# Kernel optimization log

Measured on AMD Instinct MI355X. Metric: run time of the kernel, lower is better.

Reference implementation:

```python
import jax, jax.numpy as jnp
import numpy as np

EPS = 1e-7  # K.epsilon()


def setup_inputs() -> dict:
    key = jax.random.key(0)
    k1, k2, k3, k4 = jax.random.split(key, 4)
    B, T, S = 512, 32, 2048  # batch, time_steps, seq_len
    inputs = jax.random.normal(k1, (B, T, S), dtype=jnp.float32)
    # Keras mask (float 0/1), same shape as inputs
    mask = (jax.random.uniform(k2, (B, T, S)) < 0.8).astype(jnp.float32)
    # 'uniform' keras initializer: U(-0.05, 0.05)
    W = jax.random.uniform(k3, (S, T, T), minval=-0.05, maxval=0.05, dtype=jnp.float32)
    b = jax.random.uniform(k4, (S, T), minval=-0.05, maxval=0.05, dtype=jnp.float32)
    return {"inputs": inputs, "mask": mask, "W": W, "b": b}


def reference(inputs, mask, W, b):
    # (B,T,S) -> (B,S,T), apply mask
    x = jnp.transpose(inputs, (0, 2, 1)) * jnp.transpose(mask, (0, 2, 1))
    # per-position matmul, batched over B and S (replaces the tf.scan over batch)
    z = jnp.einsum('bst,stu->bsu', x, W) + b  # (B,S,T)
    e = jnp.exp(jnp.tanh(z))
    att = e / (jnp.sum(e, axis=2, keepdims=True) + EPS)  # softmax-like over T
    return jnp.sum(att * x, axis=1)  # (B,T)
```

## Files before the change

kernel.cpp:

```cpp
#include <hip/hip_runtime.h>

#define EPS_K 1e-7f

typedef __attribute__((ext_vector_type(8)))  short          frag8;
typedef __attribute__((ext_vector_type(16))) float          accf16;
typedef __attribute__((ext_vector_type(4)))  unsigned short us4;

__device__ __forceinline__ unsigned f2bf(float f) {
  union { float f; unsigned u; } v; v.f = f;
  unsigned u = v.u;
  u += 0x7FFFu + ((u >> 16) & 1u);
  return u >> 16;
}
__device__ __forceinline__ float bf2f(unsigned short s) {
  union { unsigned u; float f; } v; v.u = ((unsigned)s) << 16;
  return v.f;
}
__device__ __forceinline__ unsigned pk_bf16(float lo, float hi) {
  return f2bf(lo) | (f2bf(hi) << 16);
}

__global__ __launch_bounds__(256) void wbf_prep(
    const float* __restrict__ Wt, unsigned short* __restrict__ Wbf)
{
  __shared__ unsigned short tile[32 * 33];
  const int s   = blockIdx.x;
  const int tid = threadIdx.x;
  {
    const int t  = tid >> 3;
    const int uc = tid & 7;
    const float4 v = *(const float4*)(Wt + s * 1024 + t * 32 + 4 * uc);
    tile[t * 33 + 4 * uc + 0] = (unsigned short)f2bf(v.x);
    tile[t * 33 + 4 * uc + 1] = (unsigned short)f2bf(v.y);
    tile[t * 33 + 4 * uc + 2] = (unsigned short)f2bf(v.z);
    tile[t * 33 + 4 * uc + 3] = (unsigned short)f2bf(v.w);
  }
  __syncthreads();
  {
    const int u  = tid >> 3;
    const int tc = tid & 7;
    uint2 d;
    d.x = (unsigned)tile[(4 * tc + 0) * 33 + u] | ((unsigned)tile[(4 * tc + 1) * 33 + u] << 16);
    d.y = (unsigned)tile[(4 * tc + 2) * 33 + u] | ((unsigned)tile[(4 * tc + 3) * 33 + u] << 16);
    *(uint2*)(Wbf + s * 1024 + u * 32 + 4 * tc) = d;
  }
}

template <bool WBF, bool USE_WS>
__global__ __launch_bounds__(256, 5) void attn_fused(
    const float* __restrict__ inp,
    const float* __restrict__ msk,
    const float* __restrict__ Wt,
    const unsigned short* __restrict__ Wbf,
    const float* __restrict__ bias,
    float* __restrict__ part,
    float* __restrict__ out)
{
  __shared__ unsigned short x_us[32 * 512];

  const int tid = threadIdx.x;
  const int st  = blockIdx.x >> 4;
  const int bg  = blockIdx.x & 15;
  const int s0  = st * 16;

  #pragma unroll
  for (int iter = 0; iter < 2; ++iter) {
    const int idx = iter * 256 + tid;
    const int sc  = idx & 3;
    const int tb  = (idx >> 2) & 3;
    const int b   = idx >> 4;
    const float* ip = inp + ((size_t)(bg * 32 + b) * 32 + 8 * tb) * 2048 + s0 + 4 * sc;
    const float* mp = msk + ((size_t)(bg * 32 + b) * 32 + 8 * tb) * 2048 + s0 + 4 * sc;
    unsigned c32[4][4];
    #pragma unroll
    for (int j2 = 0; j2 < 4; ++j2) {
      const float4 vi0 = *(const float4*)(ip + (2 * j2)     * 2048);
      const float4 vm0 = *(const float4*)(mp + (2 * j2)     * 2048);
      const float4 vi1 = *(const float4*)(ip + (2 * j2 + 1) * 2048);
      const float4 vm1 = *(const float4*)(mp + (2 * j2 + 1) * 2048);
      c32[0][j2] = pk_bf16(vi0.x * vm0.x, vi1.x * vm1.x);
      c32[1][j2] = pk_bf16(vi0.y * vm0.y, vi1.y * vm1.y);
      c32[2][j2] = pk_bf16(vi0.z * vm0.z, vi1.z * vm1.z);
      c32[3][j2] = pk_bf16(vi0.w * vm0.w, vi1.w * vm1.w);
    }
    #pragma unroll
    for (int w = 0; w < 4; ++w) {
      const int L = tb * 16 + 4 * sc + w;
      unsigned* dst = (unsigned*)(x_us + b * 512 + ((L ^ (b & 7)) * 8));
      *(uint4*)dst = make_uint4(c32[w][0], c32[w][1], c32[w][2], c32[w][3]);
    }
  }
  __syncthreads();

  const int lane = tid & 63;
  const int wv   = tid >> 6;
  const int n    = lane & 31;
  const int h    = lane >> 5;
  const int nx   = n & 7;

  float O[16];
  #pragma unroll
  for (int r = 0; r < 16; ++r) O[r] = 0.f;

  #pragma unroll
  for (int si = 0; si < 4; ++si) {
    const int sl = wv * 4 + si;
    const int s  = s0 + sl;

    frag8 a1, a2;
    if (WBF) {
      const unsigned short* wp = Wbf + s * 1024 + n * 32 + 8 * h;
      a1 = *(const frag8*)(wp);
      a2 = *(const frag8*)(wp + 16);
    } else {
      const float* Wp = Wt + s * 1024;
      #pragma unroll
      for (int j = 0; j < 8; ++j) {
        const int t1 = 8 * h + j;
        a1[j] = (short)f2bf(Wp[t1 * 32 + n]);
        a2[j] = (short)f2bf(Wp[(t1 + 16) * 32 + n]);
      }
    }

    const frag8 b1 = *(const frag8*)(x_us + n * 512 + (((h      * 16 + sl) ^ nx) * 8));
    const frag8 b2 = *(const frag8*)(x_us + n * 512 + ((((h + 2) * 16 + sl) ^ nx) * 8));

    accf16 acc;
    #pragma unroll
    for (int g = 0; g < 4; ++g) {
      const float4 bb = *(const float4*)(bias + s * 32 + 8 * g + 4 * h);
      acc[4 * g + 0] = bb.x; acc[4 * g + 1] = bb.y;
      acc[4 * g + 2] = bb.z; acc[4 * g + 3] = bb.w;
    }
    acc = __builtin_amdgcn_mfma_f32_32x32x16_bf16(a1, b1, acc, 0, 0, 0);
    acc = __builtin_amdgcn_mfma_f32_32x32x16_bf16(a2, b2, acc, 0, 0, 0);

    float e[16];
    float ps = 0.f;
    #pragma unroll
    for (int r = 0; r < 16; ++r) {
      const float z  = acc[r];
      const float e2 = __expf(2.f * z);
      const float th = 1.f - 2.f / (e2 + 1.f);
      e[r] = __expf(th);
      ps  += e[r];
    }
    const float tot = ps + __shfl_xor(ps, 32, 64);
    const float inv = 1.f / (tot + EPS_K);

    #pragma unroll
    for (int g = 0; g < 4; ++g) {
      const us4 xv = *(const us4*)(x_us + n * 512 + (((g * 16 + sl) ^ nx) * 8) + 4 * h);
      #pragma unroll
      for (int i = 0; i < 4; ++i)
        O[4 * g + i] += e[4 * g + i] * inv * bf2f(xv[i]);
    }
  }

  __syncthreads();
  float* red = (float*)x_us;
  #pragma unroll
  for (int r = 0; r < 16; ++r) {
    const int u = (r & 3) + 8 * (r >> 2) + 4 * h;
    red[wv * 1024 + n * 32 + (u ^ n)] = O[r];
  }
  __syncthreads();

  const int q0 = tid * 4;
  float4 v;
  float* vp = (float*)&v;
  #pragma unroll
  for (int i = 0; i < 4; ++i) {
    const int q = q0 + i;
    const int b = q >> 5, u = q & 31;
    float sum = 0.f;
    #pragma unroll
    for (int w = 0; w < 4; ++w) sum += red[w * 1024 + b * 32 + (u ^ b)];
    vp[i] = sum;
  }
  if (USE_WS) {
    *(float4*)(part + (size_t)st * 16384 + bg * 1024 + q0) = v;
  } else {
    float* op = out + bg * 1024 + q0;
    #pragma unroll
    for (int i = 0; i < 4; ++i) atomicAdd(op + i, vp[i]);
  }
}

__global__ __launch_bounds__(256) void reduce_part(
    const float* __restrict__ part, float* __restrict__ out)
{
  const int f = blockIdx.x * 256 + threadIdx.x;
  float s = 0.f;
  #pragma unroll 8
  for (int st = 0; st < 128; ++st) s += part[(size_t)st * 16384 + f];
  out[f] = s;
}

extern "C" void kernel_launch(void* const* d_in, const int* in_sizes, int n_in,
                              void* d_out, int out_size, void* d_ws, size_t ws_size,
                              hipStream_t stream) {
  const float* inp  = (const float*)d_in[0];
  const float* msk  = (const float*)d_in[1];
  const float* Wt   = (const float*)d_in[2];
  const float* bias = (const float*)d_in[3];
  float* out = (float*)d_out;

  const size_t part_sz = (size_t)128 * 16384 * sizeof(float);
  const size_t wbf_sz  = (size_t)2048 * 1024 * sizeof(unsigned short);

  if (ws_size >= part_sz + wbf_sz) {
    float* part = (float*)d_ws;
    unsigned short* Wbf = (unsigned short*)((char*)d_ws + part_sz);
    wbf_prep<<<dim3(2048), dim3(256), 0, stream>>>(Wt, Wbf);
    attn_fused<true, true><<<dim3(2048), dim3(256), 0, stream>>>(
        inp, msk, Wt, Wbf, bias, part, out);
    reduce_part<<<dim3(64), dim3(256), 0, stream>>>(part, out);
  } else if (ws_size >= part_sz) {
    float* part = (float*)d_ws;
    attn_fused<false, true><<<dim3(2048), dim3(256), 0, stream>>>(
        inp, msk, Wt, nullptr, bias, part, out);
    reduce_part<<<dim3(64), dim3(256), 0, stream>>>(part, out);
  } else {
    (void)hipMemsetAsync(out, 0, (size_t)out_size * sizeof(float), stream);
    attn_fused<false, false><<<dim3(2048), dim3(256), 0, stream>>>(
        inp, msk, Wt, nullptr, bias, nullptr, out);
  }
}
```

Baseline: 311.3 us.

## Retile fused attention to 32 positions x 16 batches with 16x16x32 MFMA

Each block now covers 32 sequence positions and 16 batch rows instead of 16 positions and 32 rows, and the per-position matmul uses two 16x16x32 bf16 MFMAs instead of two 32x32x16 ones. The partial-sum buffer shrinks to 64 slices, so the final reduction reads half as much data. The staging loads issue all input and mask float4 reads up front and write to a new unswizzled LDS layout. Each contiguous read along the sequence axis becomes 128 bytes instead of 64, which should improve memory coalescing. The risks are more registers held in flight and possible LDS bank conflicts, since the XOR swizzle was dropped.

After: 316.4 us. About the same (+1.7%).

```diff
diff --git a/kernel.cpp b/kernel.cpp
--- a/kernel.cpp
+++ b/kernel.cpp
@@ -2,9 +2,9 @@
 
 #define EPS_K 1e-7f
 
-typedef __attribute__((ext_vector_type(8)))  short          frag8;
-typedef __attribute__((ext_vector_type(16))) float          accf16;
-typedef __attribute__((ext_vector_type(4)))  unsigned short us4;
+typedef __attribute__((ext_vector_type(8))) short          frag8;
+typedef __attribute__((ext_vector_type(4))) float          accf4;
+typedef __attribute__((ext_vector_type(4))) unsigned short us4;
 
 __device__ __forceinline__ unsigned f2bf(float f) {
   union { float f; unsigned u; } v; v.f = f;
@@ -56,134 +56,135 @@
     float* __restrict__ part,
     float* __restrict__ out)
 {
-  __shared__ unsigned short x_us[32 * 512];
+  __shared__ unsigned short x_us[16384];
 
   const int tid = threadIdx.x;
-  const int st  = blockIdx.x >> 4;
-  const int bg  = blockIdx.x & 15;
-  const int s0  = st * 16;
+  const int st  = blockIdx.x >> 5;
+  const int bg  = blockIdx.x & 31;
+  const int s0  = st * 32;
 
   #pragma unroll
   for (int iter = 0; iter < 2; ++iter) {
     const int idx = iter * 256 + tid;
-    const int sc  = idx & 3;
-    const int tb  = (idx >> 2) & 3;
-    const int b   = idx >> 4;
-    const float* ip = inp + ((size_t)(bg * 32 + b) * 32 + 8 * tb) * 2048 + s0 + 4 * sc;
-    const float* mp = msk + ((size_t)(bg * 32 + b) * 32 + 8 * tb) * 2048 + s0 + 4 * sc;
-    unsigned c32[4][4];
-    #pragma unroll
-    for (int j2 = 0; j2 < 4; ++j2) {
-      const float4 vi0 = *(const float4*)(ip + (2 * j2)     * 2048);
-      const float4 vm0 = *(const float4*)(mp + (2 * j2)     * 2048);
-      const float4 vi1 = *(const float4*)(ip + (2 * j2 + 1) * 2048);
-      const float4 vm1 = *(const float4*)(mp + (2 * j2 + 1) * 2048);
-      c32[0][j2] = pk_bf16(vi0.x * vm0.x, vi1.x * vm1.x);
-      c32[1][j2] = pk_bf16(vi0.y * vm0.y, vi1.y * vm1.y);
-      c32[2][j2] = pk_bf16(vi0.z * vm0.z, vi1.z * vm1.z);
-      c32[3][j2] = pk_bf16(vi0.w * vm0.w, vi1.w * vm1.w);
-    }
-    #pragma unroll
-    for (int w = 0; w < 4; ++w) {
-      const int L = tb * 16 + 4 * sc + w;
-      unsigned* dst = (unsigned*)(x_us + b * 512 + ((L ^ (b & 7)) * 8));
-      *(uint4*)dst = make_uint4(c32[w][0], c32[w][1], c32[w][2], c32[w][3]);
+    const int sq  = idx & 7;
+    const int q   = (idx >> 3) & 3;
+    const int b   = idx >> 5;
+    const size_t rbase = ((size_t)(bg * 16 + b) * 32 + 8 * q) * 2048 + s0 + 4 * sq;
+    const float* ip = inp + rbase;
+    const float* mp = msk + rbase;
+    float4 vi4[8], vm4[8];
+    #pragma unroll
+    for (int j = 0; j < 8; ++j) vi4[j] = *(const float4*)(ip + (size_t)j * 2048);
+    #pragma unroll
+    for (int j = 0; j < 8; ++j) vm4[j] = *(const float4*)(mp + (size_t)j * 2048);
+    const float* vi = (const float*)vi4;
+    const float* vm = (const float*)vm4;
+    #pragma unroll
+    for (int i = 0; i < 4; ++i) {
+      uint4 c;
+      c.x = pk_bf16(vi[0 * 4 + i] * vm[0 * 4 + i], vi[1 * 4 + i] * vm[1 * 4 + i]);
+      c.y = pk_bf16(vi[2 * 4 + i] * vm[2 * 4 + i], vi[3 * 4 + i] * vm[3 * 4 + i]);
+      c.z = pk_bf16(vi[4 * 4 + i] * vm[4 * 4 + i], vi[5 * 4 + i] * vm[5 * 4 + i]);
+      c.w = pk_bf16(vi[6 * 4 + i] * vm[6 * 4 + i], vi[7 * 4 + i] * vm[7 * 4 + i]);
+      const int slot = 4 * sq + i;
+      *(uint4*)(x_us + (size_t)(slot * 64 + b * 4 + q) * 8) = c;
     }
   }
   __syncthreads();
 
   const int lane = tid & 63;
   const int wv   = tid >> 6;
-  const int n    = lane & 31;
-  const int h    = lane >> 5;
-  const int nx   = n & 7;
-
-  float O[16];
-  #pragma unroll
-  for (int r = 0; r < 16; ++r) O[r] = 0.f;
-
-  #pragma unroll
-  for (int si = 0; si < 4; ++si) {
-    const int sl = wv * 4 + si;
-    const int s  = s0 + sl;
-
-    frag8 a1, a2;
+  const int m    = lane & 15;
+  const int q    = lane >> 4;
+
+  float O[8];
+  #pragma unroll
+  for (int r = 0; r < 8; ++r) O[r] = 0.f;
+
+  #pragma unroll
+  for (int si = 0; si < 8; ++si) {
+    const int slot = wv * 8 + si;
+    const int s    = s0 + slot;
+
+    frag8 a0, a1;
     if (WBF) {
-      const unsigned short* wp = Wbf + s * 1024 + n * 32 + 8 * h;
-      a1 = *(const frag8*)(wp);
-      a2 = *(const frag8*)(wp + 16);
+      const unsigned short* wp = Wbf + s * 1024 + m * 32 + 8 * q;
+      a0 = *(const frag8*)(wp);
+      a1 = *(const frag8*)(wp + 512);
     } else {
       const float* Wp = Wt + s * 1024;
       #pragma unroll
       for (int j = 0; j < 8; ++j) {
-        const int t1 = 8 * h + j;
-        a1[j] = (short)f2bf(Wp[t1 * 32 + n]);
-        a2[j] = (short)f2bf(Wp[(t1 + 16) * 32 + n]);
+        const int t1 = 8 * q + j;
+        a0[j] = (short)f2bf(Wp[t1 * 32 + m]);
+        a1[j] = (short)f2bf(Wp[t1 * 32 + 16 + m]);
       }
     }
 
-    const frag8 b1 = *(const frag8*)(x_us + n * 512 + (((h      * 16 + sl) ^ nx) * 8));
-    const frag8 b2 = *(const frag8*)(x_us + n * 512 + ((((h + 2) * 16 + sl) ^ nx) * 8));
-
-    accf16 acc;
-    #pragma unroll
-    for (int g = 0; g < 4; ++g) {
-      const float4 bb = *(const float4*)(bias + s * 32 + 8 * g + 4 * h);
-      acc[4 * g + 0] = bb.x; acc[4 * g + 1] = bb.y;
-      acc[4 * g + 2] = bb.z; acc[4 * g + 3] = bb.w;
-    }
-    acc = __builtin_amdgcn_mfma_f32_32x32x16_bf16(a1, b1, acc, 0, 0, 0);
-    acc = __builtin_amdgcn_mfma_f32_32x32x16_bf16(a2, b2, acc, 0, 0, 0);
-
-    float e[16];
+    const frag8 bf = *(const frag8*)(x_us + (size_t)(slot * 64 + m * 4 + q) * 8);
+
+    const float4 bb0 = *(const float4*)(bias + s * 32 + 4 * q);
+    const float4 bb1 = *(const float4*)(bias + s * 32 + 16 + 4 * q);
+    accf4 acc0, acc1;
+    acc0[0] = bb0.x; acc0[1] = bb0.y; acc0[2] = bb0.z; acc0[3] = bb0.w;
+    acc1[0] = bb1.x; acc1[1] = bb1.y; acc1[2] = bb1.z; acc1[3] = bb1.w;
+    acc0 = __builtin_amdgcn_mfma_f32_16x16x32_bf16(a0, bf, acc0, 0, 0, 0);
+    acc1 = __builtin_amdgcn_mfma_f32_16x16x32_bf16(a1, bf, acc1, 0, 0, 0);
+
+    float e[8];
     float ps = 0.f;
     #pragma unroll
-    for (int r = 0; r < 16; ++r) {
-      const float z  = acc[r];
+    for (int r = 0; r < 4; ++r) {
+      const float z  = acc0[r];
       const float e2 = __expf(2.f * z);
-      const float th = 1.f - 2.f / (e2 + 1.f);
-      e[r] = __expf(th);
+      e[r] = __expf(1.f - 2.f / (e2 + 1.f));
       ps  += e[r];
     }
-    const float tot = ps + __shfl_xor(ps, 32, 64);
+    #pragma unroll
+    for (int r = 0; r < 4; ++r) {
+      const float z  = acc1[r];
+      const float e2 = __expf(2.f * z);
+      e[4 + r] = __expf(1.f - 2.f / (e2 + 1.f));
+      ps += e[4 + r];
+    }
+    const float t1s = ps + __shfl_xor(ps, 16, 64);
+    const float tot = t1s + __shfl_xor(t1s, 32, 64);
     const float inv = 1.f / (tot + EPS_K);
 
-    #pragma unroll
-    for (int g = 0; g < 4; ++g) {
-      const us4 xv = *(const us4*)(x_us + n * 512 + (((g * 16 + sl) ^ nx) * 8) + 4 * h);
-      #pragma unroll
-      for (int i = 0; i < 4; ++i)
-        O[4 * g + i] += e[4 * g + i] * inv * bf2f(xv[i]);
+    const us4 x0 = *(const us4*)(x_us + (size_t)(slot * 64 + m * 4 + (q >> 1)) * 8 + 4 * (q & 1));
+    const us4 x1 = *(const us4*)(x_us + (size_t)(slot * 64 + m * 4 + 2 + (q >> 1)) * 8 + 4 * (q & 1));
+    #pragma unroll
+    for (int r = 0; r < 4; ++r) {
+      O[r]     += e[r]     * inv * bf2f(x0[r]);
+      O[4 + r] += e[4 + r] * inv * bf2f(x1[r]);
     }
   }
 
   __syncthreads();
   float* red = (float*)x_us;
   #pragma unroll
-  for (int r = 0; r < 16; ++r) {
-    const int u = (r & 3) + 8 * (r >> 2) + 4 * h;
-    red[wv * 1024 + n * 32 + (u ^ n)] = O[r];
-  }
-  __syncthreads();
-
-  const int q0 = tid * 4;
-  float4 v;
-  float* vp = (float*)&v;
-  #pragma unroll
-  for (int i = 0; i < 4; ++i) {
-    const int q = q0 + i;
-    const int b = q >> 5, u = q & 31;
+  for (int r = 0; r < 8; ++r) {
+    const int u = (r < 4) ? (4 * q + r) : (16 + 4 * q + (r - 4));
+    red[wv * 512 + m * 32 + (u ^ m)] = O[r];
+  }
+  __syncthreads();
+
+  const int f0 = tid * 2;
+  float2 v;
+  #pragma unroll
+  for (int i = 0; i < 2; ++i) {
+    const int f = f0 + i, b = f >> 5, u = f & 31;
     float sum = 0.f;
     #pragma unroll
-    for (int w = 0; w < 4; ++w) sum += red[w * 1024 + b * 32 + (u ^ b)];
-    vp[i] = sum;
+    for (int w = 0; w < 4; ++w) sum += red[w * 512 + b * 32 + (u ^ b)];
+    (&v.x)[i] = sum;
   }
   if (USE_WS) {
-    *(float4*)(part + (size_t)st * 16384 + bg * 1024 + q0) = v;
+    *(float2*)(part + (size_t)st * 16384 + bg * 512 + f0) = v;
   } else {
-    float* op = out + bg * 1024 + q0;
-    #pragma unroll
-    for (int i = 0; i < 4; ++i) atomicAdd(op + i, vp[i]);
+    float* op = out + bg * 512 + f0;
+    atomicAdd(op, v.x);
+    atomicAdd(op + 1, v.y);
   }
 }
 
@@ -193,7 +194,7 @@
   const int f = blockIdx.x * 256 + threadIdx.x;
   float s = 0.f;
   #pragma unroll 8
-  for (int st = 0; st < 128; ++st) s += part[(size_t)st * 16384 + f];
+  for (int st = 0; st < 64; ++st) s += part[(size_t)st * 16384 + f];
   out[f] = s;
 }
 
@@ -206,7 +207,7 @@
   const float* bias = (const float*)d_in[3];
   float* out = (float*)d_out;
 
-  const size_t part_sz = (size_t)128 * 16384 * sizeof(float);
+  const size_t part_sz = (size_t)64 * 16384 * sizeof(float);
   const size_t wbf_sz  = (size_t)2048 * 1024 * sizeof(unsigned short);
 
   if (ws_size >= part_sz + wbf_sz) {
```
